# Kernel optimization log

Measured on AMD Instinct MI355X. Metric: run time of the kernel, lower is better.

## Reference

```python
import jax, jax.numpy as jnp
import numpy as np

B, F, T, D = 64, 128, 64, 256  # batch, n_features, time_length, temporalDim


def setup_inputs() -> dict:
    key = jax.random.key(0)
    ks = jax.random.split(key, 7)
    return {
        "x": jax.random.normal(ks[0], (B, F, T), dtype=jnp.float32),
        # Conv1d(1, D, 1) per timestep: weight [D,1,1] and bias [D] stacked over T -> [T, D]
        "wconv": jax.random.normal(ks[1], (T, D), dtype=jnp.float32) * 0.1,
        "bconv": jax.random.normal(ks[2], (T, D), dtype=jnp.float32) * 0.1,
        # W1: ParameterList of [D,1] -> [T, D]; b1: list of [1,F] -> [T, F]
        "w1": jax.random.normal(ks[3], (T, D), dtype=jnp.float32),
        "b1": jax.random.normal(ks[4], (T, F), dtype=jnp.float32),
        # W2: [D,1] -> [D]; b2: [1,T] -> [T]
        "w2": jax.random.normal(ks[5], (D,), dtype=jnp.float32),
        "b2": jax.random.normal(ks[6], (T,), dtype=jnp.float32),
    }


def reference(x, wconv, bconv, w1, b1, w2, b2):
    # Dropout is identity (eval mode).
    # Kernel-size-1 Conv1d over [B,1,F] == outer product of the scalar x[b,f,t] with wconv[t] + bias.
    xt = jnp.transpose(x, (0, 2, 1))                      # [B, T, F]
    sT = xt[..., None] * wconv[None, :, None, :] + bconv[None, :, None, :]  # [B, T, F, D]
    # per-step variable attention: sigmoid(sT @ W1 + b1)
    vatt = jax.nn.sigmoid(jnp.einsum("btfd,td->btf", sT, w1) + b1[None])    # [B, T, F]
    # attention-pooled per-step representation
    result = jnp.einsum("btf,btfd->btd", vatt, sT)        # [B, T, D]
    # temporal attention over steps
    tatt = jax.nn.sigmoid(jnp.einsum("btd,d->bt", result, w2) + b2[None])   # [B, T]
    out = jnp.einsum("bt,btd->bd", tatt, result)          # [B, D]
    variAtten = jnp.transpose(vatt, (0, 2, 1))            # [B, F, T]
    return out, variAtten * tatt[:, None, :]
```

## Files before the change

### kernel.cpp

```cpp
#include <hip/hip_runtime.h>
#include <math.h>

#define B 64
#define F 128
#define T 64
#define D 256

__global__ __launch_bounds__(64) void precompute_kernel(
    const float* __restrict__ wconv, const float* __restrict__ bconv,
    const float* __restrict__ w1, const float* __restrict__ w2,
    float* __restrict__ ws) {
    const int t = blockIdx.x;
    const int lane = threadIdx.x;
    const int base = t * D + lane * 4;
    const float4 wc  = *reinterpret_cast<const float4*>(wconv + base);
    const float4 bc  = *reinterpret_cast<const float4*>(bconv + base);
    const float4 w1v = *reinterpret_cast<const float4*>(w1 + base);
    const float4 w2v = *reinterpret_cast<const float4*>(w2 + lane * 4);
    float a = wc.x*w1v.x + wc.y*w1v.y + wc.z*w1v.z + wc.w*w1v.w;
    float c = bc.x*w1v.x + bc.y*w1v.y + bc.z*w1v.z + bc.w*w1v.w;
    float p = wc.x*w2v.x + wc.y*w2v.y + wc.z*w2v.z + wc.w*w2v.w;
    float q = bc.x*w2v.x + bc.y*w2v.y + bc.z*w2v.z + bc.w*w2v.w;
    #pragma unroll
    for (int off = 32; off > 0; off >>= 1) {
        a += __shfl_down(a, off);
        c += __shfl_down(c, off);
        p += __shfl_down(p, off);
        q += __shfl_down(q, off);
    }
    if (lane == 0) {
        ws[t]         = a;
        ws[T + t]     = c;
        ws[2 * T + t] = p;
        ws[3 * T + t] = q;
    }
}

__global__ __launch_bounds__(256) void main_kernel(
    const float* __restrict__ x,
    const float* __restrict__ wconv, const float* __restrict__ bconv,
    const float* __restrict__ b1, const float* __restrict__ b2,
    const float* __restrict__ ws,
    float* __restrict__ out1, float* __restrict__ out2) {

    __shared__ float vatt_s[F * T];
    __shared__ float b1_s[F * (T + 1)];
    __shared__ float s0red[4 * T], s1red[4 * T];
    __shared__ float s0_s[T], s1_s[T], tatt_s[T];

    const int b = blockIdx.x;
    const int tid = threadIdx.x;
    const int w = tid >> 6;
    const int lane = tid & 63;

    const float* xb = x + b * F * T;

    float xv[32];
    #pragma unroll
    for (int i = 0; i < 32; ++i) {
        xv[i] = xb[(w + 4 * i) * T + lane];
    }

    for (int lin = tid; lin < T * F; lin += 256) {
        const int t = lin >> 7;
        const int f = lin & (F - 1);
        b1_s[f * (T + 1) + t] = b1[lin];
    }

    const float At = ws[lane];
    const float Ct = ws[T + lane];

    __syncthreads();

    float s0 = 0.f, s1 = 0.f;
    #pragma unroll
    for (int i = 0; i < 32; ++i) {
        const int f = w + 4 * i;
        const float z = xv[i] * At + Ct + b1_s[f * (T + 1) + lane];
        const float v = 1.0f / (1.0f + __expf(-z));
        vatt_s[f * T + lane] = v;
        s0 += v;
        s1 += v * xv[i];
    }
    s0red[w * T + lane] = s0;
    s1red[w * T + lane] = s1;
    __syncthreads();

    if (tid < T) {
        const float S0 = s0red[tid] + s0red[T + tid] + s0red[2 * T + tid] + s0red[3 * T + tid];
        const float S1 = s1red[tid] + s1red[T + tid] + s1red[2 * T + tid] + s1red[3 * T + tid];
        const float Pt = ws[2 * T + tid];
        const float Qt = ws[3 * T + tid];
        const float z = S1 * Pt + S0 * Qt + b2[tid];
        const float ta = 1.0f / (1.0f + __expf(-z));
        s0_s[tid] = S0;
        s1_s[tid] = S1;
        tatt_s[tid] = ta;
    }
    __syncthreads();

    float acc = 0.f;
    #pragma unroll 16
    for (int t = 0; t < T; ++t) {
        acc += tatt_s[t] * (wconv[t * D + tid] * s1_s[t] + bconv[t * D + tid] * s0_s[t]);
    }
    out1[b * D + tid] = acc;

    float* o2 = out2 + b * F * T;
    for (int lin = tid; lin < F * T; lin += 256) {
        o2[lin] = vatt_s[lin] * tatt_s[lin & (T - 1)];
    }
}

extern "C" void kernel_launch(void* const* d_in, const int* in_sizes, int n_in,
                              void* d_out, int out_size, void* d_ws, size_t ws_size,
                              hipStream_t stream) {
    const float* x     = (const float*)d_in[0];
    const float* wconv = (const float*)d_in[1];
    const float* bconv = (const float*)d_in[2];
    const float* w1    = (const float*)d_in[3];
    const float* b1    = (const float*)d_in[4];
    const float* w2    = (const float*)d_in[5];
    const float* b2    = (const float*)d_in[6];
    float* out = (float*)d_out;
    float* ws  = (float*)d_ws;

    precompute_kernel<<<T, 64, 0, stream>>>(wconv, bconv, w1, w2, ws);
    main_kernel<<<B, 256, 0, stream>>>(x, wconv, bconv, b1, b2, ws,
                                       out, out + B * D);
}
```

Before: 73.98 us.

## Fuse precompute into main kernel and split time axis across blocks with atomics

Removes the separate precompute kernel and has each block recompute its own per-timestep dot products. The time dimension is split into chunks of 16, so the grid grows from 64 to 256 blocks, and shared memory per block shrinks by keeping vatt in registers. Partial pooled outputs are combined with atomicAdd into a buffer zeroed by a memset. The goal is more parallelism and one fewer dependent launch. The cost is redundant dot-product work per block, an extra memset, atomic contention, and float accumulation whose order is no longer fixed.

```diff
diff --git a/kernel.cpp b/kernel.cpp
--- a/kernel.cpp
+++ b/kernel.cpp
@@ -5,110 +5,109 @@
 #define F 128
 #define T 64
 #define D 256
+#define TC 16
+#define NC (T / TC)
 
-__global__ __launch_bounds__(64) void precompute_kernel(
-    const float* __restrict__ wconv, const float* __restrict__ bconv,
-    const float* __restrict__ w1, const float* __restrict__ w2,
-    float* __restrict__ ws) {
-    const int t = blockIdx.x;
-    const int lane = threadIdx.x;
-    const int base = t * D + lane * 4;
-    const float4 wc  = *reinterpret_cast<const float4*>(wconv + base);
-    const float4 bc  = *reinterpret_cast<const float4*>(bconv + base);
-    const float4 w1v = *reinterpret_cast<const float4*>(w1 + base);
-    const float4 w2v = *reinterpret_cast<const float4*>(w2 + lane * 4);
-    float a = wc.x*w1v.x + wc.y*w1v.y + wc.z*w1v.z + wc.w*w1v.w;
-    float c = bc.x*w1v.x + bc.y*w1v.y + bc.z*w1v.z + bc.w*w1v.w;
-    float p = wc.x*w2v.x + wc.y*w2v.y + wc.z*w2v.z + wc.w*w2v.w;
-    float q = bc.x*w2v.x + bc.y*w2v.y + bc.z*w2v.z + bc.w*w2v.w;
-    #pragma unroll
-    for (int off = 32; off > 0; off >>= 1) {
-        a += __shfl_down(a, off);
-        c += __shfl_down(c, off);
-        p += __shfl_down(p, off);
-        q += __shfl_down(q, off);
-    }
-    if (lane == 0) {
-        ws[t]         = a;
-        ws[T + t]     = c;
-        ws[2 * T + t] = p;
-        ws[3 * T + t] = q;
-    }
-}
-
-__global__ __launch_bounds__(256) void main_kernel(
+__global__ __launch_bounds__(256) void fused_kernel(
     const float* __restrict__ x,
     const float* __restrict__ wconv, const float* __restrict__ bconv,
-    const float* __restrict__ b1, const float* __restrict__ b2,
-    const float* __restrict__ ws,
+    const float* __restrict__ w1, const float* __restrict__ b1,
+    const float* __restrict__ w2, const float* __restrict__ b2,
     float* __restrict__ out1, float* __restrict__ out2) {
 
-    __shared__ float vatt_s[F * T];
-    __shared__ float b1_s[F * (T + 1)];
-    __shared__ float s0red[4 * T], s1red[4 * T];
-    __shared__ float s0_s[T], s1_s[T], tatt_s[T];
+    __shared__ float b1_s[F * (TC + 1)];
+    __shared__ float A_s[TC], C_s[TC], P_s[TC], Q_s[TC];
+    __shared__ float s0red[4 * TC], s1red[4 * TC];
+    __shared__ float s0_s[TC], s1_s[TC], tatt_s[TC];
 
-    const int b = blockIdx.x;
-    const int tid = threadIdx.x;
-    const int w = tid >> 6;
+    const int blk = blockIdx.x;
+    const int b  = blk & (B - 1);
+    const int c  = blk >> 6;
+    const int t0 = c * TC;
+    const int tid  = threadIdx.x;
+    const int w    = tid >> 6;
     const int lane = tid & 63;
+    const int fg   = tid >> 4;
+    const int lt   = tid & (TC - 1);
 
-    const float* xb = x + b * F * T;
+    const float* xb = x + b * F * T + t0 + lt;
+    float xv[8];
+    #pragma unroll
+    for (int i = 0; i < 8; ++i) xv[i] = xb[(fg + 16 * i) * T];
 
-    float xv[32];
     #pragma unroll
-    for (int i = 0; i < 32; ++i) {
-        xv[i] = xb[(w + 4 * i) * T + lane];
+    for (int k = 0; k < (TC * F) / 256; ++k) {
+        const int lin = tid + 256 * k;
+        const int tl  = lin >> 7;
+        const int f   = lin & (F - 1);
+        b1_s[f * (TC + 1) + tl] = b1[(t0 + tl) * F + f];
     }
 
-    for (int lin = tid; lin < T * F; lin += 256) {
-        const int t = lin >> 7;
-        const int f = lin & (F - 1);
-        b1_s[f * (T + 1) + t] = b1[lin];
+    {
+        const float4 w2v = *reinterpret_cast<const float4*>(w2 + lane * 4);
+        #pragma unroll
+        for (int j = 0; j < 4; ++j) {
+            const int tl = w * 4 + j;
+            const int base = (t0 + tl) * D + lane * 4;
+            const float4 wc  = *reinterpret_cast<const float4*>(wconv + base);
+            const float4 bc  = *reinterpret_cast<const float4*>(bconv + base);
+            const float4 w1v = *reinterpret_cast<const float4*>(w1 + base);
+            float a  = wc.x*w1v.x + wc.y*w1v.y + wc.z*w1v.z + wc.w*w1v.w;
+            float cc = bc.x*w1v.x + bc.y*w1v.y + bc.z*w1v.z + bc.w*w1v.w;
+            float p  = wc.x*w2v.x + wc.y*w2v.y + wc.z*w2v.z + wc.w*w2v.w;
+            float q  = bc.x*w2v.x + bc.y*w2v.y + bc.z*w2v.z + bc.w*w2v.w;
+            #pragma unroll
+            for (int off = 32; off > 0; off >>= 1) {
+                a  += __shfl_down(a, off);
+                cc += __shfl_down(cc, off);
+                p  += __shfl_down(p, off);
+                q  += __shfl_down(q, off);
+            }
+            if (lane == 0) { A_s[tl] = a; C_s[tl] = cc; P_s[tl] = p; Q_s[tl] = q; }
+        }
     }
-
-    const float At = ws[lane];
-    const float Ct = ws[T + lane];
-
     __syncthreads();
 
+    const float At = A_s[lt], Ct = C_s[lt];
+    float vreg[8];
     float s0 = 0.f, s1 = 0.f;
     #pragma unroll
-    for (int i = 0; i < 32; ++i) {
-        const int f = w + 4 * i;
-        const float z = xv[i] * At + Ct + b1_s[f * (T + 1) + lane];
+    for (int i = 0; i < 8; ++i) {
+        const int f = fg + 16 * i;
+        const float z = xv[i] * At + Ct + b1_s[f * (TC + 1) + lt];
         const float v = 1.0f / (1.0f + __expf(-z));
-        vatt_s[f * T + lane] = v;
+        vreg[i] = v;
         s0 += v;
         s1 += v * xv[i];
     }
-    s0red[w * T + lane] = s0;
-    s1red[w * T + lane] = s1;
+    s0 += __shfl_down(s0, 32); s1 += __shfl_down(s1, 32);
+    s0 += __shfl_down(s0, 16); s1 += __shfl_down(s1, 16);
+    if (lane < TC) { s0red[w * TC + lane] = s0; s1red[w * TC + lane] = s1; }
     __syncthreads();
 
-    if (tid < T) {
-        const float S0 = s0red[tid] + s0red[T + tid] + s0red[2 * T + tid] + s0red[3 * T + tid];
-        const float S1 = s1red[tid] + s1red[T + tid] + s1red[2 * T + tid] + s1red[3 * T + tid];
-        const float Pt = ws[2 * T + tid];
-        const float Qt = ws[3 * T + tid];
-        const float z = S1 * Pt + S0 * Qt + b2[tid];
-        const float ta = 1.0f / (1.0f + __expf(-z));
+    if (tid < TC) {
+        const float S0 = s0red[tid] + s0red[TC + tid] + s0red[2*TC + tid] + s0red[3*TC + tid];
+        const float S1 = s1red[tid] + s1red[TC + tid] + s1red[2*TC + tid] + s1red[3*TC + tid];
+        const float z  = S1 * P_s[tid] + S0 * Q_s[tid] + b2[t0 + tid];
         s0_s[tid] = S0;
         s1_s[tid] = S1;
-        tatt_s[tid] = ta;
+        tatt_s[tid] = 1.0f / (1.0f + __expf(-z));
     }
     __syncthreads();
 
     float acc = 0.f;
-    #pragma unroll 16
-    for (int t = 0; t < T; ++t) {
-        acc += tatt_s[t] * (wconv[t * D + tid] * s1_s[t] + bconv[t * D + tid] * s0_s[t]);
+    #pragma unroll
+    for (int j = 0; j < TC; ++j) {
+        const int t = t0 + j;
+        acc += tatt_s[j] * (wconv[t * D + tid] * s1_s[j] + bconv[t * D + tid] * s0_s[j]);
     }
-    out1[b * D + tid] = acc;
+    atomicAdd(out1 + b * D + tid, acc);
 
-    float* o2 = out2 + b * F * T;
-    for (int lin = tid; lin < F * T; lin += 256) {
-        o2[lin] = vatt_s[lin] * tatt_s[lin & (T - 1)];
+    float* o2 = out2 + b * F * T + t0 + lt;
+    const float ta = tatt_s[lt];
+    #pragma unroll
+    for (int i = 0; i < 8; ++i) {
+        o2[(fg + 16 * i) * T] = vreg[i] * ta;
     }
 }
 
@@ -123,9 +122,8 @@
     const float* w2    = (const float*)d_in[5];
     const float* b2    = (const float*)d_in[6];
     float* out = (float*)d_out;
-    float* ws  = (float*)d_ws;
 
-    precompute_kernel<<<T, 64, 0, stream>>>(wconv, bconv, w1, w2, ws);
-    main_kernel<<<B, 256, 0, stream>>>(x, wconv, bconv, b1, b2, ws,
-                                       out, out + B * D);
+    hipMemsetAsync(out, 0, B * D * sizeof(float), stream);
+    fused_kernel<<<B * NC, 256, 0, stream>>>(x, wconv, bconv, w1, b1, w2, b2,
+                                             out, out + B * D);
 }
```

Result: faster. 71.32 us (-3.6%).
